# Optimization experiments

Measured on AMD Instinct MI355X. Metric: run time of the kernel, lower is better.

## Reference

```python
import jax, jax.numpy as jnp
import numpy as np

NUM_HEADS = 8
EPS = 1e-6


def _edge_boost(x, density_weight):
    # x: [B, C, H, W] -> boost: [B, H*W] (per-query additive bias)
    B, C, H, W = x.shape
    sx = jnp.array([[-1., 0., 1.], [-2., 0., 2.], [-1., 0., 1.]], dtype=x.dtype)
    sy = jnp.array([[-1., -2., -1.], [0., 0., 0.], [1., 2., 1.]], dtype=x.dtype)
    feat_mean = x.mean(axis=1, keepdims=True)            # [B,1,H,W]
    kern = jnp.stack([sx, sy])[:, None]                  # [2,1,3,3] (OIHW)
    g = jax.lax.conv_general_dilated(
        feat_mean, kern, window_strides=(1, 1), padding='SAME',
        dimension_numbers=('NCHW', 'OIHW', 'NCHW'))     # [B,2,H,W]
    edge = jnp.sqrt(g[:, 0] ** 2 + g[:, 1] ** 2 + EPS)   # [B,H,W]
    return density_weight * jnp.log1p(edge.reshape(B, H * W))


def setup_inputs() -> dict:
    key = jax.random.key(0)
    k1, k2, k3 = jax.random.split(key, 3)
    B, C, H, W = 2, 256, 56, 56
    x = jax.random.normal(k1, (B, C, H, W), dtype=jnp.float32)
    Wqkv = jax.random.normal(k2, (3 * C, C), dtype=jnp.float32) * 0.02
    Wproj = jax.random.normal(k3, (C, C), dtype=jnp.float32) * 0.02
    bproj = jnp.zeros((C,), dtype=jnp.float32)
    density_weight = jnp.float32(1.0)
    return {"x": x, "Wqkv": Wqkv, "Wproj": Wproj, "bproj": bproj,
            "density_weight": density_weight}


def reference(x, Wqkv, Wproj, bproj, density_weight):
    B, C, H, W = x.shape
    h = NUM_HEADS
    d = C // h
    N = H * W
    scale = d ** -0.5

    x_flat = x.reshape(B, C, N).transpose(0, 2, 1)        # [B,N,C]
    qkv = x_flat @ Wqkv.T                                 # [B,N,3C]
    qkv = qkv.reshape(B, N, 3, h, d).transpose(2, 0, 3, 1, 4)  # [3,B,h,N,d]
    q, k, v = qkv[0], qkv[1], qkv[2]

    attn = jnp.einsum('bhqd,bhkd->bhqk', q, k) * scale    # [B,h,N,N]
    boost = _edge_boost(x, density_weight)                # [B,N]
    attn = attn + boost[:, None, :, None]                 # per-query bias, bcast over heads/keys
    attn = jax.nn.softmax(attn, axis=-1)
    # dropout is identity in eval mode

    out = jnp.einsum('bhqk,bhkd->bhqd', attn, v)          # [B,h,N,d]
    out = out.transpose(0, 2, 1, 3).reshape(B, N, C)      # [B,N,C]
    out = out @ Wproj.T + bproj
    return out.transpose(0, 2, 1).reshape(B, C, H, W)
```

## Files before the change

kernel.cpp:

```cpp
#include <hip/hip_runtime.h>
#include <hip/hip_bf16.h>
#include <math.h>

#define NQ    3136
#define CDIM  256
#define HEADS 8
#define NT    49


typedef __attribute__((ext_vector_type(8))) short short8;
typedef __attribute__((ext_vector_type(4))) float f32x4;

__device__ __forceinline__ short f2bf(float f) {
    union { float f; unsigned u; } v; v.f = f;
    unsigned r = v.u + 0x7fff + ((v.u >> 16) & 1);
    return (short)(r >> 16);
}

__device__ __forceinline__ unsigned pk_bf16(float a, float b) {
    unsigned r;
    asm("v_cvt_pk_bf16_f32 %0, %1, %2" : "=v"(r) : "v"(a), "v"(b));
    return r;
}

#define SCALE_L2E 0.25503487523f

__global__ __launch_bounds__(256) void prep(const float* __restrict__ x,
                                            const float* __restrict__ Wq,
                                            const float* __restrict__ Wp,
                                            short* __restrict__ xT,
                                            short* __restrict__ Wb,
                                            short* __restrict__ Wpb) {
    const int bx = blockIdx.x;
    const int t  = threadIdx.x;
    if (bx == 52) {
        const int wp   = blockIdx.y + 4 * blockIdx.z;
        const int base = wp * 8192 + t * 4;
        #pragma unroll
        for (int i = 0; i < 8; ++i) {
            float4 v = *(const float4*)(Wp + base + i * 1024);
            uint2 o = { pk_bf16(v.x, v.y), pk_bf16(v.z, v.w) };
            *(uint2*)(Wpb + base + i * 1024) = o;
        }
        return;
    }
    if (bx >= 49) {
        const int wb   = (bx - 49) + 3 * (blockIdx.y + 4 * blockIdx.z);
        const int base = wb * 8192 + t * 4;
        #pragma unroll
        for (int i = 0; i < 8; ++i) {
            float4 v = *(const float4*)(Wq + base + i * 1024);
            uint2 o = { pk_bf16(v.x, v.y), pk_bf16(v.z, v.w) };
            *(uint2*)(Wb + base + i * 1024) = o;
        }
        return;
    }
    __shared__ short lt[64][72];
    const int b = blockIdx.z, cb = blockIdx.y, nb = bx;
    const float* xb = x + (size_t)b * CDIM * NQ + (size_t)(cb * 64) * NQ + nb * 64;
    #pragma unroll
    for (int it = 0; it < 4; ++it) {
        const int cc = (t >> 4) + 16 * it;
        const int nn = (t & 15) * 4;
        float4 v = *(const float4*)(xb + (size_t)cc * NQ + nn);
        lt[nn + 0][cc] = f2bf(v.x);
        lt[nn + 1][cc] = f2bf(v.y);
        lt[nn + 2][cc] = f2bf(v.z);
        lt[nn + 3][cc] = f2bf(v.w);
    }
    __syncthreads();
    const int n2 = t >> 2, c2 = (t & 3) * 16;
    short* dst = xT + ((size_t)b * NQ + nb * 64 + n2) * CDIM + cb * 64 + c2;
    *(uint4*)dst       = *(const uint4*)&lt[n2][c2];
    *(uint4*)(dst + 8) = *(const uint4*)&lt[n2][c2 + 8];
}

__global__ __launch_bounds__(256) void qkv_mfma(const short* __restrict__ xT,
                                                const short* __restrict__ Wb,
                                                short* __restrict__ Qs,
                                                short* __restrict__ Kb,
                                                short* __restrict__ V4) {
    __shared__ short xs[64][40];
    __shared__ short wsm[64][40];
    __shared__ short eps[64][72];
    const int nb = blockIdx.x, jb = blockIdx.y, b = blockIdx.z;
    const int n0 = nb * 64, j0 = jb * 64;
    const int t = threadIdx.x;
    const int lane = t & 63, w = t >> 6, g = lane >> 4, ql = lane & 15;
    const int srow = t >> 2, sc = (t & 3) * 8;

    const short* xsrc = xT + ((size_t)b * NQ + n0 + srow) * CDIM + sc;
    const short* wsrc = Wb + (size_t)(j0 + srow) * CDIM + sc;

    short8 xr = *(const short8*)(xsrc);
    short8 wr = *(const short8*)(wsrc);

    f32x4 acc[4] = {};
    for (int c0 = 0; c0 < 256; c0 += 32) {
        *(short8*)&xs[srow][sc]  = xr;
        *(short8*)&wsm[srow][sc] = wr;
        __syncthreads();
        if (c0 + 32 < 256) {
            xr = *(const short8*)(xsrc + c0 + 32);
            wr = *(const short8*)(wsrc + c0 + 32);
        }
        short8 bf = *(const short8*)&wsm[16 * w + ql][8 * g];
        #pragma unroll
        for (int r = 0; r < 4; ++r) {
            short8 af = *(const short8*)&xs[16 * r + ql][8 * g];
            acc[r] = __builtin_amdgcn_mfma_f32_16x16x32_bf16(af, bf, acc[r], 0, 0, 0);
        }
        __syncthreads();
    }

    const int sect = jb >> 2;
    const int hb   = (jb & 3) * 2;
    const int jloc = 16 * w + ql;

    if (sect < 2) {
        const float sc2 = (sect == 0) ? SCALE_L2E : 1.0f;
        #pragma unroll
        for (int r = 0; r < 4; ++r)
            #pragma unroll
            for (int i = 0; i < 4; ++i)
                eps[16 * r + 4 * g + i][jloc] = f2bf(acc[r][i] * sc2);
        __syncthreads();
        short* dstb = (sect == 0) ? Qs : Kb;
        const int n2 = t >> 2, jc = (t & 3) * 16;
        const int head = hb + (jc >> 5), d0 = jc & 31;
        short* dst = dstb + ((size_t)(b * 8 + head) * NQ + n0 + n2) * 32 + d0;
        *(uint4*)dst       = *(const uint4*)&eps[n2][jc];
        *(uint4*)(dst + 8) = *(const uint4*)&eps[n2][jc + 8];
    } else {
        #pragma unroll
        for (int r = 0; r < 4; ++r)
            #pragma unroll
            for (int i = 0; i < 4; ++i)
                eps[jloc][16 * r + 4 * g + i] = f2bf(acc[r][i]);
        __syncthreads();
        const int f  = t >> 6;
        const int l2 = t & 63;
        const int gg = l2 >> 4, qq = l2 & 15;
        const int dl = ((f & 2) ? 16 : 0) + qq;
        const int ko = ((f & 1) ? 32 : 0) + 8 * gg;
        #pragma unroll
        for (int h2 = 0; h2 < 2; ++h2) {
            const uint4 val = *(const uint4*)&eps[32 * h2 + dl][ko];
            short* dst = V4 + ((((size_t)(b * 8 + hb + h2) * NT + nb) * 4 + f) * 64 + l2) * 8;
            *(uint4*)dst = val;
        }
    }
}

__global__ __launch_bounds__(256) void attn_mfma(const short* __restrict__ Qs,
                                                 const short* __restrict__ Kb,
                                                 const short* __restrict__ V4,
                                                 short* __restrict__ Ob) {
    __shared__ __align__(16) short pq[4][32][72];

    const int bid = blockIdx.x;
    const int xcd = bid & 7;
    const int ii  = bid >> 3;
    const int bh  = xcd * 2 + (ii & 1);
    const int q0  = (ii >> 1) * 64;

    const int t    = threadIdx.x;
    const int lane = t & 63;
    const int w    = t >> 6;
    const int g    = lane >> 4;
    const int ql   = lane & 15;
    const int qg   = w & 1, half = w >> 1;
    const int qbase = q0 + 32 * qg;

    const short* Qh = Qs + (size_t)bh * NQ * 32;
    const short* Kh = Kb + (size_t)bh * NQ * 32;
    const short* Vh = V4 + (size_t)bh * (NT * 2048) + (size_t)lane * 8;

    const short8 qfA = *(const short8*)(Qh + (size_t)(qbase + ql) * 32 + 8 * g);
    const short8 qfB = *(const short8*)(Qh + (size_t)(qbase + 16 + ql) * 32 + 8 * g);

    short8 ones;
    #pragma unroll
    for (int e = 0; e < 8; ++e) ones[e] = (short)0x3F80;

    const short* kp = Kh + (size_t)ql * 32 + 8 * g;

    f32x4 otA0 = {0,0,0,0}, otA1 = {0,0,0,0};
    f32x4 otB0 = {0,0,0,0}, otB1 = {0,0,0,0};
    f32x4 otlA = {0,0,0,0}, otlB = {0,0,0,0};

    const short* vt0 = Vh + half * 2048;
    short8 vc00 = *(const short8*)(vt0);
    short8 vc01 = *(const short8*)(vt0 + 512);
    short8 vc10 = *(const short8*)(vt0 + 1024);
    short8 vc11 = *(const short8*)(vt0 + 1536);

    for (int i = 0; i < 25; ++i) {
        const int cur = 2 * i + half;
        const int nxt = cur + 2;
        const int tn  = (nxt < NT) ? nxt : 48;
        const short* vtn = Vh + (size_t)tn * 2048;
        short8 vn00 = *(const short8*)(vtn);
        short8 vn01 = *(const short8*)(vtn + 512);
        short8 vn10 = *(const short8*)(vtn + 1024);
        short8 vn11 = *(const short8*)(vtn + 1536);

        if (cur < NT) {
            const int k0 = cur * 64;
            short8 kf0 = *(const short8*)(kp + (size_t)(k0 +  0) * 32);
            short8 kf1 = *(const short8*)(kp + (size_t)(k0 + 16) * 32);
            short8 kf2 = *(const short8*)(kp + (size_t)(k0 + 32) * 32);
            short8 kf3 = *(const short8*)(kp + (size_t)(k0 + 48) * 32);

            __builtin_amdgcn_s_setprio(1);
            f32x4 stA[4], stB[4];
            stA[0] = __builtin_amdgcn_mfma_f32_16x16x32_bf16(kf0, qfA, (f32x4){0,0,0,0}, 0, 0, 0);
            stB[0] = __builtin_amdgcn_mfma_f32_16x16x32_bf16(kf0, qfB, (f32x4){0,0,0,0}, 0, 0, 0);
            stA[1] = __builtin_amdgcn_mfma_f32_16x16x32_bf16(kf1, qfA, (f32x4){0,0,0,0}, 0, 0, 0);
            stB[1] = __builtin_amdgcn_mfma_f32_16x16x32_bf16(kf1, qfB, (f32x4){0,0,0,0}, 0, 0, 0);
            stA[2] = __builtin_amdgcn_mfma_f32_16x16x32_bf16(kf2, qfA, (f32x4){0,0,0,0}, 0, 0, 0);
            stB[2] = __builtin_amdgcn_mfma_f32_16x16x32_bf16(kf2, qfB, (f32x4){0,0,0,0}, 0, 0, 0);
            stA[3] = __builtin_amdgcn_mfma_f32_16x16x32_bf16(kf3, qfA, (f32x4){0,0,0,0}, 0, 0, 0);
            stB[3] = __builtin_amdgcn_mfma_f32_16x16x32_bf16(kf3, qfB, (f32x4){0,0,0,0}, 0, 0, 0);
            __builtin_amdgcn_s_setprio(0);

            float pA[16], pB[16];
            #pragma unroll
            for (int c = 0; c < 4; ++c)
                #pragma unroll
                for (int e = 0; e < 4; ++e) {
                    pA[4 * c + e] = __builtin_amdgcn_exp2f(stA[c][e]);
                    pB[4 * c + e] = __builtin_amdgcn_exp2f(stB[c][e]);
                }

            #pragma unroll
            for (int c = 0; c < 4; ++c) {
                uint2 va_ = { pk_bf16(pA[4 * c + 0], pA[4 * c + 1]),
                              pk_bf16(pA[4 * c + 2], pA[4 * c + 3]) };
                *(uint2*)&pq[w][ql][16 * c + 4 * g] = va_;
                uint2 vb_ = { pk_bf16(pB[4 * c + 0], pB[4 * c + 1]),
                              pk_bf16(pB[4 * c + 2], pB[4 * c + 3]) };
                *(uint2*)&pq[w][16 + ql][16 * c + 4 * g] = vb_;
            }
            asm volatile("s_waitcnt lgkmcnt(0)" ::: "memory");

            short8 pbA0 = *(const short8*)&pq[w][ql][8 * g];
            short8 pbA1 = *(const short8*)&pq[w][ql][32 + 8 * g];
            short8 pbB0 = *(const short8*)&pq[w][16 + ql][8 * g];
            short8 pbB1 = *(const short8*)&pq[w][16 + ql][32 + 8 * g];

            __builtin_amdgcn_s_setprio(1);
            otA0 = __builtin_amdgcn_mfma_f32_16x16x32_bf16(vc00, pbA0, otA0, 0, 0, 0);
            otA0 = __builtin_amdgcn_mfma_f32_16x16x32_bf16(vc01, pbA1, otA0, 0, 0, 0);
            otA1 = __builtin_amdgcn_mfma_f32_16x16x32_bf16(vc10, pbA0, otA1, 0, 0, 0);
            otA1 = __builtin_amdgcn_mfma_f32_16x16x32_bf16(vc11, pbA1, otA1, 0, 0, 0);
            otB0 = __builtin_amdgcn_mfma_f32_16x16x32_bf16(vc00, pbB0, otB0, 0, 0, 0);
            otB0 = __builtin_amdgcn_mfma_f32_16x16x32_bf16(vc01, pbB1, otB0, 0, 0, 0);
            otB1 = __builtin_amdgcn_mfma_f32_16x16x32_bf16(vc10, pbB0, otB1, 0, 0, 0);
            otB1 = __builtin_amdgcn_mfma_f32_16x16x32_bf16(vc11, pbB1, otB1, 0, 0, 0);
            otlA = __builtin_amdgcn_mfma_f32_16x16x32_bf16(ones, pbA0, otlA, 0, 0, 0);
            otlA = __builtin_amdgcn_mfma_f32_16x16x32_bf16(ones, pbA1, otlA, 0, 0, 0);
            otlB = __builtin_amdgcn_mfma_f32_16x16x32_bf16(ones, pbB0, otlB, 0, 0, 0);
            otlB = __builtin_amdgcn_mfma_f32_16x16x32_bf16(ones, pbB1, otlB, 0, 0, 0);
            __builtin_amdgcn_s_setprio(0);
        }

        vc00 = vn00; vc01 = vn01; vc10 = vn10; vc11 = vn11;
    }

    const float lA = otlA[0];
    const float lB = otlB[0];

    __syncthreads();
    float* mrg = (float*)&pq[0][0][0];
    if (half == 1) {
        float* pp = mrg + ((size_t)qg * 64 + lane) * 20;
        *(f32x4*)(pp + 0)  = otA0;
        *(f32x4*)(pp + 4)  = otA1;
        *(f32x4*)(pp + 8)  = otB0;
        *(f32x4*)(pp + 12) = otB1;
        pp[16] = lA; pp[17] = lB;
    }
    __syncthreads();
    if (half == 0) {
        const float* pp = mrg + ((size_t)qg * 64 + lane) * 20;
        f32x4 a0 = *(const f32x4*)(pp + 0);
        f32x4 a1 = *(const f32x4*)(pp + 4);
        f32x4 b0 = *(const f32x4*)(pp + 8);
        f32x4 b1 = *(const f32x4*)(pp + 12);
        const float invA = 1.f / (lA + pp[16]);
        const float invB = 1.f / (lB + pp[17]);
        const int b = bh >> 3, h = bh & 7;
        short* orowA = Ob + ((size_t)b * NQ + qbase + ql) * CDIM + h * 32;
        short* orowB = Ob + ((size_t)b * NQ + qbase + 16 + ql) * CDIM + h * 32;
        uint2 wA0 = { pk_bf16((otA0[0]+a0[0])*invA, (otA0[1]+a0[1])*invA),
                      pk_bf16((otA0[2]+a0[2])*invA, (otA0[3]+a0[3])*invA) };
        uint2 wA1 = { pk_bf16((otA1[0]+a1[0])*invA, (otA1[1]+a1[1])*invA),
                      pk_bf16((otA1[2]+a1[2])*invA, (otA1[3]+a1[3])*invA) };
        uint2 wB0 = { pk_bf16((otB0[0]+b0[0])*invB, (otB0[1]+b0[1])*invB),
                      pk_bf16((otB0[2]+b0[2])*invB, (otB0[3]+b0[3])*invB) };
        uint2 wB1 = { pk_bf16((otB1[0]+b1[0])*invB, (otB1[1]+b1[1])*invB),
                      pk_bf16((otB1[2]+b1[2])*invB, (otB1[3]+b1[3])*invB) };
        *(uint2*)(orowA + 4 * g)      = wA0;
        *(uint2*)(orowA + 16 + 4 * g) = wA1;
        *(uint2*)(orowB + 4 * g)      = wB0;
        *(uint2*)(orowB + 16 + 4 * g) = wB1;
    }
}

__global__ __launch_bounds__(256) void proj_mfma(const short* __restrict__ Ob,
                                                 const short* __restrict__ Wpb,
                                                 const float* __restrict__ bias,
                                                 float* __restrict__ out) {
    __shared__ short xs[32][40];
    __shared__ short wsm[64][40];
    __shared__ float eps[64][36];
    const int n0  = blockIdx.x * 32;
    const int co0 = blockIdx.y * 64;
    const int b   = blockIdx.z;
    const int t   = threadIdx.x;
    const int lane = t & 63, w = t >> 6, g = lane >> 4, ql = lane & 15;
    const int arow = (t & 127) >> 2, ac = (t & 3) * 8;
    const int brow = t >> 2,          bc = (t & 3) * 8;

    const short* asrc = Ob + ((size_t)b * NQ + n0 + arow) * CDIM + ac;
    const short* wsrc = Wpb + (size_t)(co0 + brow) * CDIM + bc;

    short8 ar = {};
    if (t < 128) ar = *(const short8*)(asrc);
    short8 wr = *(const short8*)(wsrc);

    f32x4 acc0 = {}, acc1 = {};
    for (int c0 = 0; c0 < 256; c0 += 32) {
        if (t < 128) *(short8*)&xs[arow][ac] = ar;
        *(short8*)&wsm[brow][bc] = wr;
        __syncthreads();
        if (c0 + 32 < 256) {
            if (t < 128) ar = *(const short8*)(asrc + c0 + 32);
            wr = *(const short8*)(wsrc + c0 + 32);
        }
        short8 bfr = *(const short8*)&wsm[16 * w + ql][8 * g];
        short8 af0 = *(const short8*)&xs[ql][8 * g];
        short8 af1 = *(const short8*)&xs[16 + ql][8 * g];
        acc0 = __builtin_amdgcn_mfma_f32_16x16x32_bf16(af0, bfr, acc0, 0, 0, 0);
        acc1 = __builtin_amdgcn_mfma_f32_16x16x32_bf16(af1, bfr, acc1, 0, 0, 0);
        __syncthreads();
    }

    const int jl = 16 * w + ql;
    const float bb = bias[co0 + jl];
    *(float4*)&eps[jl][4 * g]      = make_float4(acc0[0] + bb, acc0[1] + bb,
                                                 acc0[2] + bb, acc0[3] + bb);
    *(float4*)&eps[jl][16 + 4 * g] = make_float4(acc1[0] + bb, acc1[1] + bb,
                                                 acc1[2] + bb, acc1[3] + bb);
    __syncthreads();

    const int row = t >> 2, seg = (t & 3) * 8;
    float* outp = out + ((size_t)b * CDIM + co0 + row) * NQ + n0 + seg;
    *(float4*)(outp)     = *(const float4*)&eps[row][seg];
    *(float4*)(outp + 4) = *(const float4*)&eps[row][seg + 4];
}

extern "C" void kernel_launch(void* const* d_in, const int* in_sizes, int n_in,
                              void* d_out, int out_size, void* d_ws, size_t ws_size,
                              hipStream_t stream) {
    const float* x     = (const float*)d_in[0];
    const float* Wqkv  = (const float*)d_in[1];
    const float* Wproj = (const float*)d_in[2];
    const float* bproj = (const float*)d_in[3];
    float* out = (float*)d_out;

    short* xT  = (short*)d_ws;
    short* Wb  = xT + (size_t)2 * NQ * CDIM;
    short* Wpb = Wb + (size_t)768 * CDIM;
    short* Qs  = Wpb + (size_t)CDIM * CDIM;
    short* Kb  = Qs + (size_t)16 * NQ * 32;
    short* V4  = Kb + (size_t)16 * NQ * 32;
    short* Ob  = V4 + (size_t)16 * NT * 2048;

    prep<<<dim3(53, 4, 2), 256, 0, stream>>>(x, Wqkv, Wproj, xT, Wb, Wpb);
    qkv_mfma<<<dim3(49, 12, 2), 256, 0, stream>>>(xT, Wb, Qs, Kb, V4);
    attn_mfma<<<dim3(784, 1, 1), 256, 0, stream>>>(Qs, Kb, V4, Ob);
    proj_mfma<<<dim3(98, 4, 2), 256, 0, stream>>>(Ob, Wpb, bproj, out);
}
```

Measured before the change: 70.89 us.

## Split attention key range four ways per block with 32-query tiles

Each attention block now handles 32 queries instead of 64, with all four waves splitting the 49 key tiles four ways instead of two waves per query group splitting them two ways. The grid doubles to 1568 blocks and wave 0 merges three partial accumulators from shared memory before normalizing. This raises parallelism and shortens each wave's serial loop, but each block now re-reads K/V for half as many queries, and the merge step is longer.

```diff
diff --git a/kernel.cpp b/kernel.cpp
--- a/kernel.cpp
+++ b/kernel.cpp
@@ -162,22 +162,20 @@
     const int xcd = bid & 7;
     const int ii  = bid >> 3;
     const int bh  = xcd * 2 + (ii & 1);
-    const int q0  = (ii >> 1) * 64;
+    const int q0  = (ii >> 1) * 32;
 
     const int t    = threadIdx.x;
     const int lane = t & 63;
     const int w    = t >> 6;
     const int g    = lane >> 4;
     const int ql   = lane & 15;
-    const int qg   = w & 1, half = w >> 1;
-    const int qbase = q0 + 32 * qg;
 
     const short* Qh = Qs + (size_t)bh * NQ * 32;
     const short* Kh = Kb + (size_t)bh * NQ * 32;
     const short* Vh = V4 + (size_t)bh * (NT * 2048) + (size_t)lane * 8;
 
-    const short8 qfA = *(const short8*)(Qh + (size_t)(qbase + ql) * 32 + 8 * g);
-    const short8 qfB = *(const short8*)(Qh + (size_t)(qbase + 16 + ql) * 32 + 8 * g);
+    const short8 qfA = *(const short8*)(Qh + (size_t)(q0 + ql) * 32 + 8 * g);
+    const short8 qfB = *(const short8*)(Qh + (size_t)(q0 + 16 + ql) * 32 + 8 * g);
 
     short8 ones;
     #pragma unroll
@@ -189,16 +187,16 @@
     f32x4 otB0 = {0,0,0,0}, otB1 = {0,0,0,0};
     f32x4 otlA = {0,0,0,0}, otlB = {0,0,0,0};
 
-    const short* vt0 = Vh + half * 2048;
+    const short* vt0 = Vh + (size_t)w * 2048;
     short8 vc00 = *(const short8*)(vt0);
     short8 vc01 = *(const short8*)(vt0 + 512);
     short8 vc10 = *(const short8*)(vt0 + 1024);
     short8 vc11 = *(const short8*)(vt0 + 1536);
 
-    for (int i = 0; i < 25; ++i) {
-        const int cur = 2 * i + half;
-        const int nxt = cur + 2;
-        const int tn  = (nxt < NT) ? nxt : 48;
+    for (int i = 0; i < 13; ++i) {
+        const int cur = 4 * i + w;
+        const int nxt = cur + 4;
+        const int tn  = (nxt < NT) ? nxt : w;
         const short* vtn = Vh + (size_t)tn * 2048;
         short8 vn00 = *(const short8*)(vtn);
         short8 vn01 = *(const short8*)(vtn + 512);
@@ -273,8 +271,8 @@
 
     __syncthreads();
     float* mrg = (float*)&pq[0][0][0];
-    if (half == 1) {
-        float* pp = mrg + ((size_t)qg * 64 + lane) * 20;
+    if (w > 0) {
+        float* pp = mrg + ((size_t)(w - 1) * 64 + lane) * 20;
         *(f32x4*)(pp + 0)  = otA0;
         *(f32x4*)(pp + 4)  = otA1;
         *(f32x4*)(pp + 8)  = otB0;
@@ -282,25 +280,31 @@
         pp[16] = lA; pp[17] = lB;
     }
     __syncthreads();
-    if (half == 0) {
-        const float* pp = mrg + ((size_t)qg * 64 + lane) * 20;
-        f32x4 a0 = *(const f32x4*)(pp + 0);
-        f32x4 a1 = *(const f32x4*)(pp + 4);
-        f32x4 b0 = *(const f32x4*)(pp + 8);
-        f32x4 b1 = *(const f32x4*)(pp + 12);
-        const float invA = 1.f / (lA + pp[16]);
-        const float invB = 1.f / (lB + pp[17]);
+    if (w == 0) {
+        f32x4 sA0 = otA0, sA1 = otA1, sB0 = otB0, sB1 = otB1;
+        float LA = lA, LB = lB;
+        #pragma unroll
+        for (int u = 0; u < 3; ++u) {
+            const float* pp = mrg + ((size_t)u * 64 + lane) * 20;
+            sA0 += *(const f32x4*)(pp + 0);
+            sA1 += *(const f32x4*)(pp + 4);
+            sB0 += *(const f32x4*)(pp + 8);
+            sB1 += *(const f32x4*)(pp + 12);
+            LA += pp[16]; LB += pp[17];
+        }
+        const float invA = 1.f / LA;
+        const float invB = 1.f / LB;
         const int b = bh >> 3, h = bh & 7;
-        short* orowA = Ob + ((size_t)b * NQ + qbase + ql) * CDIM + h * 32;
-        short* orowB = Ob + ((size_t)b * NQ + qbase + 16 + ql) * CDIM + h * 32;
-        uint2 wA0 = { pk_bf16((otA0[0]+a0[0])*invA, (otA0[1]+a0[1])*invA),
-                      pk_bf16((otA0[2]+a0[2])*invA, (otA0[3]+a0[3])*invA) };
-        uint2 wA1 = { pk_bf16((otA1[0]+a1[0])*invA, (otA1[1]+a1[1])*invA),
-                      pk_bf16((otA1[2]+a1[2])*invA, (otA1[3]+a1[3])*invA) };
-        uint2 wB0 = { pk_bf16((otB0[0]+b0[0])*invB, (otB0[1]+b0[1])*invB),
-                      pk_bf16((otB0[2]+b0[2])*invB, (otB0[3]+b0[3])*invB) };
-        uint2 wB1 = { pk_bf16((otB1[0]+b1[0])*invB, (otB1[1]+b1[1])*invB),
-                      pk_bf16((otB1[2]+b1[2])*invB, (otB1[3]+b1[3])*invB) };
+        short* orowA = Ob + ((size_t)b * NQ + q0 + ql) * CDIM + h * 32;
+        short* orowB = Ob + ((size_t)b * NQ + q0 + 16 + ql) * CDIM + h * 32;
+        uint2 wA0 = { pk_bf16(sA0[0] * invA, sA0[1] * invA),
+                      pk_bf16(sA0[2] * invA, sA0[3] * invA) };
+        uint2 wA1 = { pk_bf16(sA1[0] * invA, sA1[1] * invA),
+                      pk_bf16(sA1[2] * invA, sA1[3] * invA) };
+        uint2 wB0 = { pk_bf16(sB0[0] * invB, sB0[1] * invB),
+                      pk_bf16(sB0[2] * invB, sB0[3] * invB) };
+        uint2 wB1 = { pk_bf16(sB1[0] * invB, sB1[1] * invB),
+                      pk_bf16(sB1[2] * invB, sB1[3] * invB) };
         *(uint2*)(orowA + 4 * g)      = wA0;
         *(uint2*)(orowA + 16 + 4 * g) = wA1;
         *(uint2*)(orowB + 4 * g)      = wB0;
@@ -380,6 +384,6 @@
 
     prep<<<dim3(53, 4, 2), 256, 0, stream>>>(x, Wqkv, Wproj, xT, Wb, Wpb);
     qkv_mfma<<<dim3(49, 12, 2), 256, 0, stream>>>(xT, Wb, Qs, Kb, V4);
-    attn_mfma<<<dim3(784, 1, 1), 256, 0, stream>>>(Qs, Kb, V4, Ob);
+    attn_mfma<<<dim3(1568, 1, 1), 256, 0, stream>>>(Qs, Kb, V4, Ob);
     proj_mfma<<<dim3(98, 4, 2), 256, 0, stream>>>(Ob, Wpb, bproj, out);
 }
```

New measurement: 66.48 us. 6.2% less time.
